# Optimization experiments

Hardware: AMD Instinct MI355X
Metric: run time of the kernel (lower is better)

Reference implementation:

```python
import jax, jax.numpy as jnp
import numpy as np

EC = 32        # pos-embed channels per coordinate (gno_embed_channels)
MAXP = 10000.0 # gno_embed_max_positions


def sin_embed(c):
    # c: [N, D] coords in [0,1] -> [N, D*EC] transformer-style sinusoidal embedding
    half = EC // 2
    freqs = MAXP ** (jnp.arange(half, dtype=jnp.float32) / half)
    ang = c[..., None] * freqs                       # [N, D, half]
    emb = jnp.concatenate([jnp.sin(ang), jnp.cos(ang)], axis=-1)  # [N, D, EC]
    return emb.reshape(c.shape[0], -1)


def mlp(h, layers):
    n = len(layers)
    for i, (W, b) in enumerate(layers):
        h = h @ W + b
        if i < n - 1:
            h = jax.nn.gelu(h)
    return h


def gno(y, xq, f_y, idx, layers, lift, reduction):
    # y: [n_y,3] source coords, xq: [n_x,3] query coords, f_y: [n_y,C_f], idx: [n_x,K]
    ye, xe = sin_embed(y), sin_embed(xq)
    K = idx.shape[1]
    ef = jnp.concatenate(
        [ye[idx], jnp.broadcast_to(xe[:, None, :], (xq.shape[0], K, xe.shape[-1]))], axis=-1)
    k = mlp(ef, layers)                              # [n_x, K, C] kernel values
    f = f_y if lift is None else f_y @ lift[0] + lift[1]
    msg = k * f[idx]                                 # gathered features modulated by kernel
    return msg.mean(axis=1) if reduction == 'mean' else msg.sum(axis=1)


def spectral_conv(v, w):
    # v: [1,X,Y,Z,C]; w: [4,m,m,m,C,C,2] (4 corner blocks, real/imag stacked)
    m = w.shape[2]
    wc = w[..., 0] + 1j * w[..., 1]
    vf = jnp.fft.rfftn(v, axes=(1, 2, 3))
    out = jnp.zeros_like(vf)
    corners = [(slice(0, m), slice(0, m)), (slice(0, m), slice(-m, None)),
               (slice(-m, None), slice(0, m)), (slice(-m, None), slice(-m, None))]
    for i, (sx, sy) in enumerate(corners):
        blk = jnp.einsum('bxyzi,xyzio->bxyzo', vf[:, sx, sy, :m, :], wc[i])
        out = out.at[:, sx, sy, :m, :].set(blk)
    return jnp.fft.irfftn(out, s=v.shape[1:4], axes=(1, 2, 3))


def _forward(input_geom, latent_queries, output_queries, x,
             in_lift_w, in_lift_b,
             in_k_w0, in_k_b0, in_k_w1, in_k_b1, in_k_w2, in_k_b2, in_k_w3, in_k_b3,
             lift_w0, lift_b0, lift_w1, lift_b1,
             spec_w, skip_w, gate_w, gate_b, cmlp_w0, cmlp_b0, cmlp_w1, cmlp_b1,
             out_k_w0, out_k_b0, out_k_w1, out_k_b1, out_k_w2, out_k_b2,
             proj_w0, proj_b0, proj_w1, proj_b1,
             in_idx, out_idx):
    grid = latent_queries.shape[:-1]
    flat_lq = latent_queries.reshape(-1, latent_queries.shape[-1])
    # --- input GNO: point cloud -> latent grid (mean reduction) ---
    in_layers = [(in_k_w0, in_k_b0), (in_k_w1, in_k_b1), (in_k_w2, in_k_b2), (in_k_w3, in_k_b3)]
    in_p = gno(input_geom, flat_lq, x, in_idx, in_layers, (in_lift_w, in_lift_b), 'mean')
    h = in_p.reshape((1,) + grid + (in_p.shape[-1],))
    # --- lifting ChannelMLP (2 layers) ---
    h = jax.nn.gelu(h @ lift_w0 + lift_b0) @ lift_w1 + lift_b1
    # --- FNO blocks ---
    for l in range(spec_w.shape[0]):
        v_fno = spectral_conv(h, spec_w[l])
        v_skip = h @ skip_w[l]                       # linear skip
        a = jax.nn.gelu(v_fno + v_skip)
        gate = a * gate_w[l] + gate_b[l]             # soft-gating skip
        m_ = jax.nn.gelu(a @ cmlp_w0[l] + cmlp_b0[l]) @ cmlp_w1[l] + cmlp_b1[l]
        h = jax.nn.gelu(m_ + gate)
    x_latent = h.reshape(-1, h.shape[-1])            # [nx*ny*nz, C]
    # --- output GNO: latent grid -> output queries (sum reduction) ---
    out_layers = [(out_k_w0, out_k_b0), (out_k_w1, out_k_b1), (out_k_w2, out_k_b2)]
    out_eval = gno(flat_lq, output_queries, x_latent, out_idx, out_layers, None, 'sum')
    out = out_eval[None]                             # [1, n_out, C]
    # --- projection ChannelMLP ---
    return jax.nn.gelu(out @ proj_w0 + proj_b0) @ proj_w1 + proj_b1


def setup_inputs() -> dict:
    key = jax.random.key(0)
    ks = jax.random.split(key, 24)
    N_IN, N_OUT, G, K = 100000, 30000, 32, 10
    C_IN, H = 3, 64
    KIN = 2 * 3 * EC  # 192: concat of two per-point embeddings

    def w(k, shape, fan):
        return jax.random.normal(k, shape, jnp.float32) / np.sqrt(fan)

    lin = jnp.linspace(0.0, 1.0, G)
    gx, gy, gz = jnp.meshgrid(lin, lin, lin, indexing='ij')
    d = {
        'input_geom': jax.random.uniform(ks[0], (N_IN, 3), jnp.float32),
        'latent_queries': jnp.stack([gx, gy, gz], axis=-1),
        'output_queries': jax.random.uniform(ks[1], (N_OUT, 3), jnp.float32),
        'x': jax.random.normal(ks[2], (N_IN, C_IN), jnp.float32),
        'in_lift_w': w(ks[3], (C_IN, H), C_IN), 'in_lift_b': jnp.zeros((H,)),
        'in_k_w0': w(ks[4], (KIN, 80), KIN), 'in_k_b0': jnp.zeros((80,)),
        'in_k_w1': w(ks[5], (80, 80), 80), 'in_k_b1': jnp.zeros((80,)),
        'in_k_w2': w(ks[6], (80, 80), 80), 'in_k_b2': jnp.zeros((80,)),
        'in_k_w3': w(ks[7], (80, H), 80), 'in_k_b3': jnp.zeros((H,)),
        'lift_w0': w(ks[8], (H, 128), H), 'lift_b0': jnp.zeros((128,)),
        'lift_w1': w(ks[9], (128, H), 128), 'lift_b1': jnp.zeros((H,)),
        'spec_w': jax.random.normal(ks[10], (4, 4, 8, 8, 8, H, H, 2), jnp.float32) * 0.02,
        'skip_w': w(ks[11], (4, H, H), H),
        'gate_w': jnp.ones((4, H)), 'gate_b': jnp.zeros((4, H)),
        'cmlp_w0': w(ks[12], (4, H, 128), H), 'cmlp_b0': jnp.zeros((4, 128)),
        'cmlp_w1': w(ks[13], (4, 128, H), 128), 'cmlp_b1': jnp.zeros((4, H)),
        'out_k_w0': w(ks[14], (KIN, 512), KIN), 'out_k_b0': jnp.zeros((512,)),
        'out_k_w1': w(ks[15], (512, 256), 512), 'out_k_b1': jnp.zeros((256,)),
        'out_k_w2': w(ks[16], (256, H), 256), 'out_k_b2': jnp.zeros((H,)),
        'proj_w0': w(ks[17], (H, 256), H), 'proj_b0': jnp.zeros((256,)),
        'proj_w1': w(ks[18], (256, 1), 256), 'proj_b1': jnp.zeros((1,)),
        'in_idx': jax.random.randint(ks[19], (G ** 3, K), 0, N_IN),
        'out_idx': jax.random.randint(ks[20], (N_OUT, K), 0, G ** 3),
    }
    return d


def reference(input_geom, latent_queries, output_queries, x,
              in_lift_w, in_lift_b,
              in_k_w0, in_k_b0, in_k_w1, in_k_b1, in_k_w2, in_k_b2, in_k_w3, in_k_b3,
              lift_w0, lift_b0, lift_w1, lift_b1,
              spec_w, skip_w, gate_w, gate_b, cmlp_w0, cmlp_b0, cmlp_w1, cmlp_b1,
              out_k_w0, out_k_b0, out_k_w1, out_k_b1, out_k_w2, out_k_b2,
              proj_w0, proj_b0, proj_w1, proj_b1,
              in_idx, out_idx):
    return _forward(input_geom, latent_queries, output_queries, x,
                    in_lift_w, in_lift_b,
                    in_k_w0, in_k_b0, in_k_w1, in_k_b1, in_k_w2, in_k_b2, in_k_w3, in_k_b3,
                    lift_w0, lift_b0, lift_w1, lift_b1,
                    spec_w, skip_w, gate_w, gate_b, cmlp_w0, cmlp_b0, cmlp_w1, cmlp_b1,
                    out_k_w0, out_k_b0, out_k_w1, out_k_b1, out_k_w2, out_k_b2,
                    proj_w0, proj_b0, proj_w1, proj_b1,
                    in_idx, out_idx)
```

## Files before the change

kernel.cpp:

```cpp
#include <hip/hip_runtime.h>
#include <math.h>

#define N_IN   100000
#define N_LQ   32768
#define N_OUT  30000
#define KNB    10

typedef _Float16 h8 __attribute__((ext_vector_type(8)));
typedef _Float16 h4 __attribute__((ext_vector_type(4)));
typedef float    v4f __attribute__((ext_vector_type(4)));

__device__ __forceinline__ float gelu_f(float x){
  float t = 0.79788456080286536f * (x + 0.044715f*x*x*x);
  t = fminf(fmaxf(t, -15.f), 15.f);
  float e = __expf(2.f*t);
  float th = __fdividef(e - 1.f, e + 1.f);
  return 0.5f*x*(1.f + th);
}

__global__ void k_twiddle(float* __restrict__ twc, float* __restrict__ tws){
  int t = threadIdx.x;
  if(t < 32){
    double a = (double)t * 0.19634954084936207;
    twc[t] = (float)cos(a);
    tws[t] = (float)sin(a);
  }
}

__global__ void k_prep(const float* __restrict__ okw1, const float* __restrict__ okw2,
                       const float* __restrict__ ikw1, const float* __restrict__ ikw2,
                       const float* __restrict__ ikw3,
                       _Float16* W1h, _Float16* W1l, _Float16* W2h, _Float16* W2l,
                       _Float16* I1h, _Float16* I1l, _Float16* I2h, _Float16* I2l,
                       _Float16* I3h, _Float16* I3l)
{
  int idx = blockIdx.x*256 + threadIdx.x;
  if(idx < 512*256){
    int k = idx>>8, n = idx&255;
    float v = okw1[idx];
    _Float16 hi = (_Float16)v;
    W1h[n*512+k] = hi; W1l[n*512+k] = (_Float16)((v-(float)hi)*2048.f);
  }
  if(idx < 256*64){
    int k = idx>>6, n = idx&63;
    float v = okw2[idx];
    _Float16 hi = (_Float16)v;
    W2h[n*256+k] = hi; W2l[n*256+k] = (_Float16)((v-(float)hi)*2048.f);
  }
  if(idx < 6400){
    int n = idx/80, k = idx - n*80;
    float v = ikw1[k*80+n];
    _Float16 hi = (_Float16)v;
    I1h[n*80+k] = hi; I1l[n*80+k] = (_Float16)((v-(float)hi)*2048.f);
    float v2 = ikw2[k*80+n];
    _Float16 hi2 = (_Float16)v2;
    I2h[n*80+k] = hi2; I2l[n*80+k] = (_Float16)((v2-(float)hi2)*2048.f);
  }
  if(idx < 5120){
    int n = idx/80, k = idx - n*80;
    float v = ikw3[k*64+n];
    _Float16 hi = (_Float16)v;
    I3h[n*80+k] = hi; I3l[n*80+k] = (_Float16)((v-(float)hi)*2048.f);
  }
}

__global__ void k_lift_in(const float* __restrict__ x, const float* __restrict__ w,
                          const float* __restrict__ b, float* __restrict__ f){
  int i = blockIdx.x*256 + threadIdx.x;
  if(i >= N_IN*64) return;
  int p = i>>6, c = i&63;
  float v = b[c];
  v = fmaf(x[p*3+0], w[c],      v);
  v = fmaf(x[p*3+1], w[64+c],   v);
  v = fmaf(x[p*3+2], w[128+c],  v);
  f[i] = v;
}

template<int COLS, bool BIAS>
__global__ __launch_bounds__(256) void k_embed_partial(
    const float* __restrict__ coords, int npts,
    const float* __restrict__ W, int roff,
    const float* __restrict__ bias, float* __restrict__ outp)
{
  __shared__ float emb[96*8];
  int p0 = blockIdx.x*8;
  int t  = threadIdx.x;
  for(int w = t; w < 384; w += 256){
    int pl = w / 48, s = w - pl*48;
    int d = s >> 4, fi = s & 15;
    int p = p0 + pl;
    float cd = (p < npts) ? coords[(size_t)p*3 + d] : 0.f;
    double f = exp((double)fi * 0.5756462732485115);
    double a = (double)cd * f;
    double sn, cs; sincos(a, &sn, &cs);
    emb[((d<<5)+fi)*8 + pl]      = (float)sn;
    emb[((d<<5)+16+fi)*8 + pl]   = (float)cs;
  }
  __syncthreads();
  for(int c = t; c < COLS; c += 256){
    float acc[8];
    float bb = BIAS ? bias[c] : 0.f;
    #pragma unroll
    for(int u=0;u<8;u++) acc[u] = bb;
    for(int i=0;i<96;i++){
      float wv = W[(size_t)(roff+i)*COLS + c];
      const float* ep = &emb[i*8];
      float4 e0 = *(const float4*)ep;
      float4 e1 = *(const float4*)(ep+4);
      acc[0]=fmaf(e0.x,wv,acc[0]); acc[1]=fmaf(e0.y,wv,acc[1]);
      acc[2]=fmaf(e0.z,wv,acc[2]); acc[3]=fmaf(e0.w,wv,acc[3]);
      acc[4]=fmaf(e1.x,wv,acc[4]); acc[5]=fmaf(e1.y,wv,acc[5]);
      acc[6]=fmaf(e1.z,wv,acc[6]); acc[7]=fmaf(e1.w,wv,acc[7]);
    }
    #pragma unroll
    for(int u=0;u<8;u++){
      int p = p0+u;
      if(p < npts) outp[(size_t)p*COLS + c] = acc[u];
    }
  }
}

#define GI_HAHI 0
#define GI_HALO 5632
#define GI_WHI  11264
#define GI_WLO  14464
__global__ __launch_bounds__(256,2) void k_gino(
    const float* __restrict__ Ain, const float* __restrict__ Bin,
    const float* __restrict__ f_in, const int* __restrict__ iidx,
    const _Float16* __restrict__ I1h, const _Float16* __restrict__ I1l, const float* __restrict__ b1,
    const _Float16* __restrict__ I2h, const _Float16* __restrict__ I2l, const float* __restrict__ b2,
    const _Float16* __restrict__ I3h, const _Float16* __restrict__ I3l, const float* __restrict__ b3,
    float* __restrict__ in_p)
{
  __shared__ _Float16 SG[17664];
  __shared__ int js[64]; __shared__ int qs[64];
  int t = threadIdx.x;
  int wid = t>>6, lane = t&63, quad = lane>>4, lm = lane&15;
  int et0 = blockIdx.x*64;
  if(t<64){ js[t] = iidx[et0+t]; qs[t] = (et0+t)/KNB; }
  __syncthreads();

  {
    int e = t>>2, k4 = t&3;
    size_t ja = (size_t)js[e]*80, qa = (size_t)qs[e]*80;
    #pragma unroll
    for(int u=0;u<3;u++){
      int kl = k4*8 + u*32;
      if(kl < 80){
        float4 a0 = *(const float4*)(Ain + ja + kl);
        float4 a1 = *(const float4*)(Ain + ja + kl + 4);
        float4 c0 = *(const float4*)(Bin + qa + kl);
        float4 c1 = *(const float4*)(Bin + qa + kl + 4);
        float vv[8] = {a0.x+c0.x, a0.y+c0.y, a0.z+c0.z, a0.w+c0.w,
                       a1.x+c1.x, a1.y+c1.y, a1.z+c1.z, a1.w+c1.w};
        h8 hh, ll;
        #pragma unroll
        for(int q8=0;q8<8;q8++){
          float g = gelu_f(vv[q8]);
          _Float16 hi = (_Float16)g;
          hh[q8] = hi; ll[q8] = (_Float16)((g-(float)hi)*2048.f);
        }
        *(h8*)&SG[GI_HAHI + e*88 + kl] = hh;
        *(h8*)&SG[GI_HALO + e*88 + kl] = ll;
      }
    }
  }

  const float inv = 4.8828125e-4f;
  const _Float16* whp[3] = {I1h, I2h, I3h};
  const _Float16* wlp[3] = {I1l, I2l, I3l};
  const float*    bsp[3] = {b1, b2, b3};
  v4f aH[5], aL[5];

  for(int l=0;l<3;l++){
    int NT = (l==2)?4:5;
    const _Float16* wh = whp[l];
    const _Float16* wl = wlp[l];
    #pragma unroll
    for(int n=0;n<5;n++){ aH[n] = (v4f)(0.f); aL[n] = (v4f)(0.f); }
    for(int c=0;c<3;c++){
      int kb = c*32;
      int per = (c==2)?2:4;
      int units = NT*16*per;
      __syncthreads();
      for(int u=t; u<units; u+=256){
        int n = u/per, kh = (u - n*per)*8;
        float4 rh = *(const float4*)(wh + n*80 + kb + kh);
        float4 rl = *(const float4*)(wl + n*80 + kb + kh);
        *(float4*)&SG[GI_WHI + n*40 + kh] = rh;
        *(float4*)&SG[GI_WLO + n*40 + kh] = rl;
      }
      __syncthreads();
      int arow = (wid*16+lm)*88;
      if(c<2){
        h8 ah = *(const h8*)&SG[GI_HAHI + arow + kb + quad*8];
        h8 al = *(const h8*)&SG[GI_HALO + arow + kb + quad*8];
        for(int n=0;n<NT;n++){
          int brow = (n*16+lm)*40;
          h8 bh = *(const h8*)&SG[GI_WHI + brow + quad*8];
          h8 bl = *(const h8*)&SG[GI_WLO + brow + quad*8];
          aH[n] = __builtin_amdgcn_mfma_f32_16x16x32_f16(ah, bh, aH[n], 0,0,0);
          aL[n] = __builtin_amdgcn_mfma_f32_16x16x32_f16(ah, bl, aL[n], 0,0,0);
          aL[n] = __builtin_amdgcn_mfma_f32_16x16x32_f16(al, bh, aL[n], 0,0,0);
        }
      } else {
        h4 ah = *(const h4*)&SG[GI_HAHI + arow + 64 + quad*4];
        h4 al = *(const h4*)&SG[GI_HALO + arow + 64 + quad*4];
        for(int n=0;n<NT;n++){
          int brow = (n*16+lm)*40;
          h4 bh = *(const h4*)&SG[GI_WHI + brow + quad*4];
          h4 bl = *(const h4*)&SG[GI_WLO + brow + quad*4];
          aH[n] = __builtin_amdgcn_mfma_f32_16x16x16f16(ah, bh, aH[n], 0,0,0);
          aL[n] = __builtin_amdgcn_mfma_f32_16x16x16f16(ah, bl, aL[n], 0,0,0);
          aL[n] = __builtin_amdgcn_mfma_f32_16x16x16f16(al, bh, aL[n], 0,0,0);
        }
      }
    }
    if(l<2){
      for(int n=0;n<NT;n++){
        float bb = bsp[l][n*16+lm];
        #pragma unroll
        for(int reg=0;reg<4;reg++){
          int e = wid*16 + quad*4 + reg;
          float v = aH[n][reg] + aL[n][reg]*inv + bb;
          v = gelu_f(v);
          _Float16 hi = (_Float16)v;
          SG[GI_HAHI + e*88 + n*16+lm] = hi;
          SG[GI_HALO + e*88 + n*16+lm] = (_Float16)((v-(float)hi)*2048.f);
        }
      }
    } else {
      for(int n=0;n<NT;n++){
        int col = n*16+lm;
        float bb = bsp[2][col];
        #pragma unroll
        for(int reg=0;reg<4;reg++){
          int e = wid*16 + quad*4 + reg;
          float v = aH[n][reg] + aL[n][reg]*inv + bb;
          v *= f_in[(size_t)js[e]*64 + col] * 0.1f;
          atomicAdd(&in_p[(size_t)qs[e]*64 + col], v);
        }
      }
    }
  }
}

__global__ __launch_bounds__(256,2) void k_ogno(
    const float* __restrict__ Aout, const float* __restrict__ Bout,
    const int* __restrict__ oidx,
    const _Float16* __restrict__ W1h, const _Float16* __restrict__ W1l,
    const float* __restrict__ b1,
    const _Float16* __restrict__ W2h, const _Float16* __restrict__ W2l,
    const float* __restrict__ b2,
    const float* __restrict__ xlat, float* __restrict__ outev, int eEnd)
{
  __shared__ _Float16 SH[33792];
  __shared__ int js[64]; __shared__ int qs[64];
  int t = threadIdx.x;
  int wid = t>>6, lane = t&63, quad = lane>>4, lm = lane&15;
  int et0 = blockIdx.x*64;
  if(t<64){
    int ec = et0+t; if(ec >= eEnd) ec = eEnd-1;
    js[t] = oidx[ec]; qs[t] = ec/KNB;
  }
  __syncthreads();

  v4f accH[4][4], accL[4][4];
  #pragma unroll
  for(int m=0;m<4;m++)
    #pragma unroll
    for(int n=0;n<4;n++){ accH[m][n] = (v4f)(0.f); accL[m][n] = (v4f)(0.f); }

  int se = t>>2, skl = (t&3)*8;
  const float* pa = Aout + (size_t)js[se]*512 + skl;
  const float* pb = Bout + (size_t)qs[se]*512 + skl;

  float4 cA0 = *(const float4*)(pa);
  float4 cA1 = *(const float4*)(pa+4);
  float4 cB0 = *(const float4*)(pb);
  float4 cB1 = *(const float4*)(pb+4);

  #pragma unroll 1
  for(int kk=0; kk<512; kk+=32){
    {
      float vv[8] = {cA0.x+cB0.x, cA0.y+cB0.y, cA0.z+cB0.z, cA0.w+cB0.w,
                     cA1.x+cB1.x, cA1.y+cB1.y, cA1.z+cB1.z, cA1.w+cB1.w};
      h8 hh, ll;
      #pragma unroll
      for(int q8=0;q8<8;q8++){
        float g = gelu_f(vv[q8]);
        _Float16 hi = (_Float16)g;
        hh[q8] = hi; ll[q8] = (_Float16)((g-(float)hi)*2048.f);
      }
      *(h8*)&SH[se*32 + skl] = hh;
      *(h8*)&SH[2048 + se*32 + skl] = ll;
    }
    if(kk < 480){
      cA0 = *(const float4*)(pa + kk + 32);
      cA1 = *(const float4*)(pa + kk + 36);
      cB0 = *(const float4*)(pb + kk + 32);
      cB1 = *(const float4*)(pb + kk + 36);
    }
    __syncthreads();
    h8 ah[4], al[4], bh[4], bl[4];
    #pragma unroll
    for(int m=0;m<4;m++){
      ah[m] = *(const h8*)&SH[(m*16+lm)*32 + quad*8];
      al[m] = *(const h8*)&SH[2048 + (m*16+lm)*32 + quad*8];
    }
    #pragma unroll
    for(int n=0;n<4;n++){
      size_t off = (size_t)((wid*4+n)*16+lm)*512 + kk + quad*8;
      bh[n] = *(const h8*)(W1h + off);
      bl[n] = *(const h8*)(W1l + off);
    }
    #pragma unroll
    for(int n=0;n<4;n++)
      #pragma unroll
      for(int m=0;m<4;m++)
        accH[m][n] = __builtin_amdgcn_mfma_f32_16x16x32_f16(ah[m], bh[n], accH[m][n], 0,0,0);
    #pragma unroll
    for(int n=0;n<4;n++)
      #pragma unroll
      for(int m=0;m<4;m++)
        accL[m][n] = __builtin_amdgcn_mfma_f32_16x16x32_f16(ah[m], bl[n], accL[m][n], 0,0,0);
    #pragma unroll
    for(int n=0;n<4;n++)
      #pragma unroll
      for(int m=0;m<4;m++)
        accL[m][n] = __builtin_amdgcn_mfma_f32_16x16x32_f16(al[m], bh[n], accL[m][n], 0,0,0);
    __syncthreads();
  }

  const float inv = 4.8828125e-4f;
  #pragma unroll
  for(int n=0;n<4;n++){
    int col = (wid*4+n)*16 + lm;
    float bb = b1[col];
    #pragma unroll
    for(int m=0;m<4;m++){
      #pragma unroll
      for(int reg=0;reg<4;reg++){
        int e = m*16 + quad*4 + reg;
        float v = accH[m][n][reg] + accL[m][n][reg]*inv + bb;
        v = gelu_f(v);
        _Float16 hi = (_Float16)v;
        SH[e*264 + col] = hi;
        SH[16896 + e*264 + col] = (_Float16)((v-(float)hi)*2048.f);
      }
    }
  }
  __syncthreads();

  v4f acc2H[4], acc2L[4];
  #pragma unroll
  for(int m=0;m<4;m++){ acc2H[m] = (v4f)(0.f); acc2L[m] = (v4f)(0.f); }
  int n2 = wid*16 + lm;
  #pragma unroll
  for(int c=0;c<8;c++){
    int ksub = c*32;
    size_t woff = (size_t)n2*256 + ksub + quad*8;
    h8 bh2 = *(const h8*)(W2h + woff);
    h8 bl2 = *(const h8*)(W2l + woff);
    #pragma unroll
    for(int m=0;m<4;m++){
      h8 a2h = *(const h8*)&SH[(m*16+lm)*264 + ksub + quad*8];
      h8 a2l = *(const h8*)&SH[16896 + (m*16+lm)*264 + ksub + quad*8];
      acc2H[m] = __builtin_amdgcn_mfma_f32_16x16x32_f16(a2h, bh2, acc2H[m], 0,0,0);
      acc2L[m] = __builtin_amdgcn_mfma_f32_16x16x32_f16(a2h, bl2, acc2L[m], 0,0,0);
      acc2L[m] = __builtin_amdgcn_mfma_f32_16x16x32_f16(a2l, bh2, acc2L[m], 0,0,0);
    }
  }

  float bb2 = b2[n2];
  #pragma unroll
  for(int m=0;m<4;m++){
    #pragma unroll
    for(int reg=0;reg<4;reg++){
      int e = m*16 + quad*4 + reg;
      int eg = et0 + e;
      if(eg < eEnd){
        float v = acc2H[m][reg] + acc2L[m][reg]*inv + bb2;
        v *= xlat[(size_t)js[e]*64 + n2];
        atomicAdd(&outev[(size_t)qs[e]*64 + n2], v);
      }
    }
  }
}

__global__ __launch_bounds__(256) void k_mlp_plain(const float* __restrict__ X,
    const float* __restrict__ W0, const float* __restrict__ b0,
    const float* __restrict__ W1, const float* __restrict__ b1,
    float* __restrict__ Y)
{
  __shared__ float xt[64*16];
  __shared__ float ht[128*16];
  int t = threadIdx.x, r0 = blockIdx.x*16;
  for(int w=t; w<1024; w+=256){ int r=w>>6, c=w&63; xt[c*16+r] = X[(size_t)(r0+r)*64+c]; }
  __syncthreads();
  {
    int hc = t & 127, rg = t >> 7;
    float acc[8]; float bb = b0[hc];
    #pragma unroll
    for(int u=0;u<8;u++) acc[u]=bb;
    for(int i=0;i<64;i++){
      float wv = W0[i*128+hc];
      const float* xp = &xt[i*16 + rg*8];
      float4 x0 = *(const float4*)xp; float4 x1 = *(const float4*)(xp+4);
      acc[0]=fmaf(x0.x,wv,acc[0]); acc[1]=fmaf(x0.y,wv,acc[1]);
      acc[2]=fmaf(x0.z,wv,acc[2]); acc[3]=fmaf(x0.w,wv,acc[3]);
      acc[4]=fmaf(x1.x,wv,acc[4]); acc[5]=fmaf(x1.y,wv,acc[5]);
      acc[6]=fmaf(x1.z,wv,acc[6]); acc[7]=fmaf(x1.w,wv,acc[7]);
    }
    #pragma unroll
    for(int u=0;u<8;u++) ht[hc*16 + rg*8 + u] = gelu_f(acc[u]);
  }
  __syncthreads();
  {
    int oc = t & 63, rg = t >> 6;
    float acc2[4]; float bb = b1[oc];
    #pragma unroll
    for(int u=0;u<4;u++) acc2[u]=bb;
    for(int i=0;i<128;i++){
      float wv = W1[i*64+oc];
      float4 h4v = *(const float4*)&ht[i*16 + rg*4];
      acc2[0]=fmaf(h4v.x,wv,acc2[0]); acc2[1]=fmaf(h4v.y,wv,acc2[1]);
      acc2[2]=fmaf(h4v.z,wv,acc2[2]); acc2[3]=fmaf(h4v.w,wv,acc2[3]);
    }
    #pragma unroll
    for(int u=0;u<4;u++) Y[(size_t)(r0+rg*4+u)*64 + oc] = acc2[u];
  }
}

__global__ __launch_bounds__(256) void k_mlp_gated(const float* __restrict__ X,
    const float* __restrict__ W0, const float* __restrict__ b0,
    const float* __restrict__ W1, const float* __restrict__ b1,
    const float* __restrict__ gwp, const float* __restrict__ gbp,
    float* __restrict__ Y)
{
  __shared__ float xt[64*16];
  __shared__ float ht[128*16];
  int t = threadIdx.x, r0 = blockIdx.x*16;
  for(int w=t; w<1024; w+=256){ int r=w>>6, c=w&63; xt[c*16+r] = X[(size_t)(r0+r)*64+c]; }
  __syncthreads();
  {
    int hc = t & 127, rg = t >> 7;
    float acc[8]; float bb = b0[hc];
    #pragma unroll
    for(int u=0;u<8;u++) acc[u]=bb;
    for(int i=0;i<64;i++){
      float wv = W0[i*128+hc];
      const float* xp = &xt[i*16 + rg*8];
      float4 x0 = *(const float4*)xp; float4 x1 = *(const float4*)(xp+4);
      acc[0]=fmaf(x0.x,wv,acc[0]); acc[1]=fmaf(x0.y,wv,acc[1]);
      acc[2]=fmaf(x0.z,wv,acc[2]); acc[3]=fmaf(x0.w,wv,acc[3]);
      acc[4]=fmaf(x1.x,wv,acc[4]); acc[5]=fmaf(x1.y,wv,acc[5]);
      acc[6]=fmaf(x1.z,wv,acc[6]); acc[7]=fmaf(x1.w,wv,acc[7]);
    }
    #pragma unroll
    for(int u=0;u<8;u++) ht[hc*16 + rg*8 + u] = gelu_f(acc[u]);
  }
  __syncthreads();
  {
    int oc = t & 63, rg = t >> 6;
    float acc2[4]; float bb = b1[oc];
    #pragma unroll
    for(int u=0;u<4;u++) acc2[u]=bb;
    for(int i=0;i<128;i++){
      float wv = W1[i*64+oc];
      float4 h4v = *(const float4*)&ht[i*16 + rg*4];
      acc2[0]=fmaf(h4v.x,wv,acc2[0]); acc2[1]=fmaf(h4v.y,wv,acc2[1]);
      acc2[2]=fmaf(h4v.z,wv,acc2[2]); acc2[3]=fmaf(h4v.w,wv,acc2[3]);
    }
    float gwv = gwp[oc], gbv = gbp[oc];
    #pragma unroll
    for(int u=0;u<4;u++){
      int r = rg*4+u;
      float a = xt[oc*16 + r];
      Y[(size_t)(r0+r)*64 + oc] = gelu_f(acc2[u] + fmaf(a, gwv, gbv));
    }
  }
}

__global__ void k_fz_fwd(const float* __restrict__ h, const float* __restrict__ twc,
                         const float* __restrict__ tws, float* __restrict__ Fr, float* __restrict__ Fi){
  int idx = blockIdx.x*256 + threadIdx.x;
  int c = idx&63, kz=(idx>>6)&7, y=(idx>>9)&31, x=idx>>14;
  const float* hp = h + ((size_t)(x*32+y)*32)*64 + c;
  float re=0.f, im=0.f;
  for(int z=0; z<32; z++){
    float v = hp[(size_t)z*64];
    int k = (kz*z)&31;
    re = fmaf(v, twc[k], re);
    im = fmaf(-v, tws[k], im);
  }
  Fr[idx]=re; Fi[idx]=im;
}

__global__ void k_fy_fwd(const float* __restrict__ Ar, const float* __restrict__ Ai,
                         const float* __restrict__ twc, const float* __restrict__ tws,
                         float* __restrict__ Fr, float* __restrict__ Fi){
  int idx = blockIdx.x*256 + threadIdx.x;
  int c = idx&63, kz=(idx>>6)&7, my=(idx>>9)&15, x=idx>>13;
  int ky = my<8 ? my : my+16;
  const float* pr = Ar + ((size_t)(x*32)*8+kz)*64 + c;
  const float* pi = Ai + ((size_t)(x*32)*8+kz)*64 + c;
  float re=0.f, im=0.f;
  for(int y=0;y<32;y++){
    float a = pr[(size_t)y*512], b = pi[(size_t)y*512];
    int k = (ky*y)&31; float cs=twc[k], sn=tws[k];
    re += a*cs + b*sn;
    im += b*cs - a*sn;
  }
  Fr[idx]=re; Fi[idx]=im;
}

__global__ void k_fx_fwd(const float* __restrict__ Ar, const float* __restrict__ Ai,
                         const float* __restrict__ twc, const float* __restrict__ tws,
                         float* __restrict__ Fr, float* __restrict__ Fi){
  int idx = blockIdx.x*256 + threadIdx.x;
  int c = idx&63, kz=(idx>>6)&7, my=(idx>>9)&15, mx=idx>>13;
  int kx = mx<8 ? mx : mx+16;
  const float* pr = Ar + ((size_t)my*8+kz)*64 + c;
  const float* pi = Ai + ((size_t)my*8+kz)*64 + c;
  float re=0.f, im=0.f;
  for(int x=0;x<32;x++){
    float a = pr[(size_t)x*8192], b = pi[(size_t)x*8192];
    int k = (kx*x)&31; float cs=twc[k], sn=tws[k];
    re += a*cs + b*sn;
    im += b*cs - a*sn;
  }
  Fr[idx]=re; Fi[idx]=im;
}

__global__ void k_smm(const float* __restrict__ Fr, const float* __restrict__ Fi,
                      const float* __restrict__ wlayer,
                      float* __restrict__ Gr, float* __restrict__ Gi){
  int t = threadIdx.x;
  int sub = t>>6, c = t&63;
  int mp = blockIdx.x*4 + sub;
  int kz = mp&7, my=(mp>>3)&15, mx=mp>>7;
  int corner = ((mx>=8)?2:0) | ((my>=8)?1:0);
  int kxp = mx&7, kyp = my&7;
  const float* wp = wlayer + (size_t)(((corner*8+kxp)*8+kyp)*8+kz)*8192;
  __shared__ float fre[4][64], fim[4][64];
  fre[sub][c] = Fr[(size_t)mp*64+c];
  fim[sub][c] = Fi[(size_t)mp*64+c];
  __syncthreads();
  float are=0.f, aim=0.f;
  for(int i=0;i<64;i++){
    float2 wv = *(const float2*)&wp[(size_t)(i*64+c)*2];
    float a = fre[sub][i], b = fim[sub][i];
    are += a*wv.x - b*wv.y;
    aim += a*wv.y + b*wv.x;
  }
  Gr[(size_t)mp*64+c] = are;
  Gi[(size_t)mp*64+c] = aim;
}

__global__ void k_fx_inv(const float* __restrict__ Ar, const float* __restrict__ Ai,
                         const float* __restrict__ twc, const float* __restrict__ tws,
                         float* __restrict__ Fr, float* __restrict__ Fi){
  int idx = blockIdx.x*256 + threadIdx.x;
  int c = idx&63, kz=(idx>>6)&7, my=(idx>>9)&15, x=idx>>13;
  float re=0.f, im=0.f;
  for(int mx=0;mx<16;mx++){
    int kx = mx<8 ? mx : mx+16;
    int k = (kx*x)&31; float cs=twc[k], sn=tws[k];
    float a = Ar[(size_t)((mx*16+my)*8+kz)*64+c];
    float b = Ai[(size_t)((mx*16+my)*8+kz)*64+c];
    re += a*cs - b*sn;
    im += a*sn + b*cs;
  }
  Fr[idx]=re; Fi[idx]=im;
}

__global__ void k_fy_inv(const float* __restrict__ Ar, const float* __restrict__ Ai,
                         const float* __restrict__ twc, const float* __restrict__ tws,
                         float* __restrict__ Fr, float* __restrict__ Fi){
  int idx = blockIdx.x*256 + threadIdx.x;
  int c = idx&63, kz=(idx>>6)&7, y=(idx>>9)&31, x=idx>>14;
  float re=0.f, im=0.f;
  for(int my=0;my<16;my++){
    int ky = my<8 ? my : my+16;
    int k = (ky*y)&31; float cs=twc[k], sn=tws[k];
    float a = Ar[(size_t)((x*16+my)*8+kz)*64+c];
    float b = Ai[(size_t)((x*16+my)*8+kz)*64+c];
    re += a*cs - b*sn;
    im += a*sn + b*cs;
  }
  Fr[idx]=re; Fi[idx]=im;
}

__global__ void k_fz_inv_skip(const float* __restrict__ G2re, const float* __restrict__ G2im,
    const float* __restrict__ h, const float* __restrict__ twc, const float* __restrict__ tws,
    const float* __restrict__ sw, float* __restrict__ a_out)
{
  __shared__ float hrow[4][64];
  int t = threadIdx.x; int c = t&63; int pl = t>>6;
  int p = blockIdx.x*4 + pl;
  int z = p & 31; int xy = p >> 5;
  hrow[pl][c] = h[(size_t)p*64 + c];
  __syncthreads();
  const float* gr = G2re + (size_t)(xy*8)*64 + c;
  const float* gi = G2im + (size_t)(xy*8)*64 + c;
  float acc = gr[0];
  #pragma unroll
  for(int kz=1;kz<8;kz++){
    int k = (kz*z)&31;
    acc += 2.f*(gr[(size_t)kz*64]*twc[k] - gi[(size_t)kz*64]*tws[k]);
  }
  float vfno = acc * (1.f/32768.f);
  float vskip = 0.f;
  for(int i=0;i<64;i++) vskip = fmaf(hrow[pl][i], sw[i*64+c], vskip);
  a_out[(size_t)p*64+c] = gelu_f(vfno + vskip);
}

__global__ __launch_bounds__(256) void k_proj(const float* __restrict__ outev,
    const float* __restrict__ pw0, const float* __restrict__ pb0,
    const float* __restrict__ pw1, const float* __restrict__ pb1,
    float* __restrict__ outp)
{
  __shared__ float msg[8][64];
  __shared__ float red[8][4];
  int t = threadIdx.x; int q0 = blockIdx.x*8;
  for(int w=t; w<512; w+=256){
    int qq=w>>6, o=w&63; int q=q0+qq;
    msg[qq][o] = (q<N_OUT) ? outev[(size_t)q*64+o] : 0.f;
  }
  __syncthreads();
  float p[8]; float bb = pb0[t];
  #pragma unroll
  for(int qq=0;qq<8;qq++) p[qq]=bb;
  for(int o=0;o<64;o++){
    float wv = pw0[o*256+t];
    #pragma unroll
    for(int qq=0;qq<8;qq++) p[qq] = fmaf(msg[qq][o], wv, p[qq]);
  }
  float w1v = pw1[t];
  int lane = t & 63, wid = t >> 6;
  #pragma unroll
  for(int qq=0;qq<8;qq++){
    float v = gelu_f(p[qq]) * w1v;
    for(int d=32; d>=1; d>>=1) v += __shfl_down(v, d, 64);
    if(lane==0) red[qq][wid]=v;
  }
  __syncthreads();
  if(t<8){
    int q = q0+t;
    if(q<N_OUT) outp[q] = red[t][0]+red[t][1]+red[t][2]+red[t][3] + pb1[0];
  }
}

extern "C" void kernel_launch(void* const* d_in, const int* in_sizes, int n_in,
                              void* d_out, int out_size, void* d_ws, size_t ws_size,
                              hipStream_t stream)
{
  (void)in_sizes; (void)n_in; (void)out_size; (void)ws_size;
  const float* geom = (const float*)d_in[0];
  const float* latq = (const float*)d_in[1];
  const float* outq = (const float*)d_in[2];
  const float* xin  = (const float*)d_in[3];
  const float* ilw  = (const float*)d_in[4];
  const float* ilb  = (const float*)d_in[5];
  const float* ikw0 = (const float*)d_in[6];
  const float* ikb0 = (const float*)d_in[7];
  const float* ikw1 = (const float*)d_in[8];
  const float* ikb1 = (const float*)d_in[9];
  const float* ikw2 = (const float*)d_in[10];
  const float* ikb2 = (const float*)d_in[11];
  const float* ikw3 = (const float*)d_in[12];
  const float* ikb3 = (const float*)d_in[13];
  const float* lw0  = (const float*)d_in[14];
  const float* lb0  = (const float*)d_in[15];
  const float* lw1  = (const float*)d_in[16];
  const float* lb1  = (const float*)d_in[17];
  const float* specw= (const float*)d_in[18];
  const float* skw  = (const float*)d_in[19];
  const float* gw   = (const float*)d_in[20];
  const float* gb   = (const float*)d_in[21];
  const float* cw0  = (const float*)d_in[22];
  const float* cb0  = (const float*)d_in[23];
  const float* cw1  = (const float*)d_in[24];
  const float* cb1  = (const float*)d_in[25];
  const float* okw0 = (const float*)d_in[26];
  const float* okb0 = (const float*)d_in[27];
  const float* okw1 = (const float*)d_in[28];
  const float* okb1 = (const float*)d_in[29];
  const float* okw2 = (const float*)d_in[30];
  const float* okb2 = (const float*)d_in[31];
  const float* pw0  = (const float*)d_in[32];
  const float* pb0  = (const float*)d_in[33];
  const float* pw1  = (const float*)d_in[34];
  const float* pb1  = (const float*)d_in[35];
  const int* iidx = (const int*)d_in[36];
  const int* oidx = (const int*)d_in[37];
  float* outp = (float*)d_out;
  float* ws = (float*)d_ws;

  size_t off = 0;
  float* F_IN = ws + off; off += (size_t)N_IN*64;
  float* AIN  = ws + off; off += (size_t)N_IN*80;
  float* BIN_ = ws + off; off += (size_t)N_LQ*80;
  float* AOUT = ws + off; off += (size_t)N_LQ*512;
  float* BOUT = ws + off; off += (size_t)N_OUT*512;
  float* HBUF = ws + off; off += (size_t)N_LQ*64;
  float* ABUF = ws + off; off += (size_t)N_LQ*64;
  float* FZr = ws+off; off+=524288; float* FZi = ws+off; off+=524288;
  float* FYr = ws+off; off+=262144; float* FYi = ws+off; off+=262144;
  float* FXr = ws+off; off+=131072; float* FXi = ws+off; off+=131072;
  float* GMr = ws+off; off+=131072; float* GMi = ws+off; off+=131072;
  float* G1r = ws+off; off+=262144; float* G1i = ws+off; off+=262144;
  float* G2r = ws+off; off+=524288; float* G2i = ws+off; off+=524288;
  float* OUTEV = ws+off; off += (size_t)N_OUT*64;
  float* TWC = ws+off; off+=32; float* TWS = ws+off; off+=32;
  off = (off + 3) & ~(size_t)3;
  _Float16* P = (_Float16*)(ws + off);
  _Float16 *W1h = P,          *W1l = P+131072;
  _Float16 *W2h = P+262144,   *W2l = P+278528;
  _Float16 *I1h = P+294912,   *I1l = P+301312;
  _Float16 *I2h = P+307712,   *I2l = P+314112;
  _Float16 *I3h = P+320512,   *I3l = P+325632;

  k_twiddle<<<1, 64, 0, stream>>>(TWC, TWS);
  k_prep<<<512, 256, 0, stream>>>(okw1, okw2, ikw1, ikw2, ikw3,
                                  W1h, W1l, W2h, W2l, I1h, I1l, I2h, I2l, I3h, I3l);
  k_lift_in<<<(N_IN*64)/256, 256, 0, stream>>>(xin, ilw, ilb, F_IN);
  k_embed_partial<80,false><<<N_IN/8, 256, 0, stream>>>(geom, N_IN, ikw0, 0, (const float*)nullptr, AIN);
  k_embed_partial<80,true ><<<N_LQ/8, 256, 0, stream>>>(latq, N_LQ, ikw0, 96, ikb0, BIN_);
  k_embed_partial<512,false><<<N_LQ/8, 256, 0, stream>>>(latq, N_LQ, okw0, 0, (const float*)nullptr, AOUT);
  k_embed_partial<512,true ><<<(N_OUT+7)/8, 256, 0, stream>>>(outq, N_OUT, okw0, 96, okb0, BOUT);

  hipMemsetAsync(HBUF, 0, (size_t)N_LQ*64*sizeof(float), stream);
  k_gino<<<(N_LQ*KNB)/64, 256, 0, stream>>>(AIN, BIN_, F_IN, iidx,
                                            I1h, I1l, ikb1, I2h, I2l, ikb2, I3h, I3l, ikb3, HBUF);
  k_mlp_plain<<<N_LQ/16, 256, 0, stream>>>(HBUF, lw0, lb0, lw1, lb1, HBUF);

  for(int l=0;l<4;l++){
    k_fz_fwd<<<2048,256,0,stream>>>(HBUF, TWC, TWS, FZr, FZi);
    k_fy_fwd<<<1024,256,0,stream>>>(FZr, FZi, TWC, TWS, FYr, FYi);
    k_fx_fwd<<<512,256,0,stream>>>(FYr, FYi, TWC, TWS, FXr, FXi);
    k_smm<<<512,256,0,stream>>>(FXr, FXi, specw + (size_t)l*16777216, GMr, GMi);
    k_fx_inv<<<1024,256,0,stream>>>(GMr, GMi, TWC, TWS, G1r, G1i);
    k_fy_inv<<<2048,256,0,stream>>>(G1r, G1i, TWC, TWS, G2r, G2i);
    k_fz_inv_skip<<<8192,256,0,stream>>>(G2r, G2i, HBUF, TWC, TWS, skw + (size_t)l*4096, ABUF);
    k_mlp_gated<<<N_LQ/16,256,0,stream>>>(ABUF, cw0 + (size_t)l*8192, cb0 + l*128,
                                          cw1 + (size_t)l*8192, cb1 + l*64,
                                          gw + l*64, gb + l*64, HBUF);
  }

  hipMemsetAsync(OUTEV, 0, (size_t)N_OUT*64*sizeof(float), stream);
  k_ogno<<<(N_OUT*KNB + 63)/64, 256, 0, stream>>>(AOUT, BOUT, oidx,
                                                  W1h, W1l, okb1, W2h, W2l, okb2,
                                                  HBUF, OUTEV, N_OUT*KNB);
  k_proj<<<(N_OUT+7)/8, 256, 0, stream>>>(OUTEV, pw0, pb0, pw1, pb1, outp);
}
```

Measured before the change: 1.861 ms.

## Double-buffer LDS tile in output GNO loop and use LDS-only barriers

```diff
diff --git a/kernel.cpp b/kernel.cpp
--- a/kernel.cpp
+++ b/kernel.cpp
@@ -16,6 +16,11 @@
   float e = __expf(2.f*t);
   float th = __fdividef(e - 1.f, e + 1.f);
   return 0.5f*x*(1.f + th);
+}
+
+__device__ __forceinline__ void barrier_lds(){
+  __builtin_amdgcn_s_waitcnt(0xC07F);
+  __builtin_amdgcn_s_barrier();
 }
 
 __global__ void k_twiddle(float* __restrict__ twc, float* __restrict__ tws){
@@ -138,7 +143,7 @@
   int wid = t>>6, lane = t&63, quad = lane>>4, lm = lane&15;
   int et0 = blockIdx.x*64;
   if(t<64){ js[t] = iidx[et0+t]; qs[t] = (et0+t)/KNB; }
-  __syncthreads();
+  barrier_lds();
 
   {
     int e = t>>2, k4 = t&3;
@@ -182,7 +187,7 @@
       int kb = c*32;
       int per = (c==2)?2:4;
       int units = NT*16*per;
-      __syncthreads();
+      barrier_lds();
       for(int u=t; u<units; u+=256){
         int n = u/per, kh = (u - n*per)*8;
         float4 rh = *(const float4*)(wh + n*80 + kb + kh);
@@ -190,7 +195,7 @@
         *(float4*)&SG[GI_WHI + n*40 + kh] = rh;
         *(float4*)&SG[GI_WLO + n*40 + kh] = rl;
       }
-      __syncthreads();
+      barrier_lds();
       int arow = (wid*16+lm)*88;
       if(c<2){
         h8 ah = *(const h8*)&SG[GI_HAHI + arow + kb + quad*8];
@@ -263,7 +268,7 @@
     int ec = et0+t; if(ec >= eEnd) ec = eEnd-1;
     js[t] = oidx[ec]; qs[t] = ec/KNB;
   }
-  __syncthreads();
+  barrier_lds();
 
   v4f accH[4][4], accL[4][4];
   #pragma unroll
@@ -282,6 +287,7 @@
 
   #pragma unroll 1
   for(int kk=0; kk<512; kk+=32){
+    int base = ((kk>>5)&1)*5120;
     {
       float vv[8] = {cA0.x+cB0.x, cA0.y+cB0.y, cA0.z+cB0.z, cA0.w+cB0.w,
                      cA1.x+cB1.x, cA1.y+cB1.y, cA1.z+cB1.z, cA1.w+cB1.w};
@@ -292,28 +298,29 @@
         _Float16 hi = (_Float16)g;
         hh[q8] = hi; ll[q8] = (_Float16)((g-(float)hi)*2048.f);
       }
-      *(h8*)&SH[se*32 + skl] = hh;
-      *(h8*)&SH[2048 + se*32 + skl] = ll;
-    }
+      *(h8*)&SH[base + se*40 + skl] = hh;
+      *(h8*)&SH[base + 2560 + se*40 + skl] = ll;
+    }
+    barrier_lds();
     if(kk < 480){
       cA0 = *(const float4*)(pa + kk + 32);
       cA1 = *(const float4*)(pa + kk + 36);
       cB0 = *(const float4*)(pb + kk + 32);
       cB1 = *(const float4*)(pb + kk + 36);
     }
-    __syncthreads();
-    h8 ah[4], al[4], bh[4], bl[4];
-    #pragma unroll
-    for(int m=0;m<4;m++){
-      ah[m] = *(const h8*)&SH[(m*16+lm)*32 + quad*8];
-      al[m] = *(const h8*)&SH[2048 + (m*16+lm)*32 + quad*8];
-    }
+    h8 bh[4], bl[4];
     #pragma unroll
     for(int n=0;n<4;n++){
       size_t off = (size_t)((wid*4+n)*16+lm)*512 + kk + quad*8;
       bh[n] = *(const h8*)(W1h + off);
       bl[n] = *(const h8*)(W1l + off);
     }
+    h8 ah[4], al[4];
+    #pragma unroll
+    for(int m=0;m<4;m++){
+      ah[m] = *(const h8*)&SH[base + (m*16+lm)*40 + quad*8];
+      al[m] = *(const h8*)&SH[base + 2560 + (m*16+lm)*40 + quad*8];
+    }
     #pragma unroll
     for(int n=0;n<4;n++)
       #pragma unroll
@@ -329,8 +336,8 @@
       #pragma unroll
       for(int m=0;m<4;m++)
         accL[m][n] = __builtin_amdgcn_mfma_f32_16x16x32_f16(al[m], bh[n], accL[m][n], 0,0,0);
-    __syncthreads();
-  }
+  }
+  barrier_lds();
 
   const float inv = 4.8828125e-4f;
   #pragma unroll
@@ -350,7 +357,7 @@
       }
     }
   }
-  __syncthreads();
+  barrier_lds();
 
   v4f acc2H[4], acc2L[4];
   #pragma unroll
```

Result: no change. 1.873 ms (+0.6%).
